# Optimization experiments

Measured on AMD Instinct MI355X. Metric: run time of the kernel, lower is better.

The kernel has to match this reference:

```python
import jax, jax.numpy as jnp
import numpy as np

B, C, H, W = 32, 64, 32, 32
N = H * W  # 1024 spatial positions


def setup_inputs() -> dict:
    key = jax.random.key(0)
    ks = jax.random.split(key, 7)
    s_c = 1.0 / np.sqrt(C)
    s_n = 1.0 / np.sqrt(N)
    return {
        "x": jax.random.normal(ks[0], (B, C, H, W), dtype=jnp.float32),
        "w_phi": jax.random.normal(ks[1], (C, C), dtype=jnp.float32) * s_c,
        "w_theta": jax.random.normal(ks[2], (C, C), dtype=jnp.float32) * s_c,
        "w_g": jax.random.normal(ks[3], (C, C), dtype=jnp.float32) * s_c,
        "w_mask": jax.random.normal(ks[4], (C, C), dtype=jnp.float32) * s_c,
        "w_mv": jax.random.normal(ks[5], (C, C), dtype=jnp.float32) * s_c,
        "w_mk": jax.random.normal(ks[6], (N, N), dtype=jnp.float32) * s_n,
    }


def reference(x, w_phi, w_theta, w_g, w_mask, w_mv, w_mk):
    b, c, h, w = x.shape
    n = h * w
    xf = x.reshape(b, c, n)  # [b, c, N]
    # 1x1 convs == channel GEMMs (weight layout [out, in])
    phi = jnp.einsum("oc,bcn->bon", w_phi, xf)      # [b, c, N]
    theta = jnp.einsum("oc,bcn->bno", w_theta, xf)  # [b, N, c]
    g = jnp.einsum("oc,bcn->bno", w_g, xf)          # [b, N, c]
    # mv: Linear(c, c) on last dim of g  (y = g @ W^T)
    g = jnp.einsum("bnc,dc->bnd", g, w_mv)
    # theta @ phi -> [b, N, N]
    att = jnp.einsum("bnc,bcm->bnm", theta, phi)
    # mk: Linear(N, N) on last dim
    att = jnp.einsum("bnm,km->bnk", att, w_mk)
    # softmax over dim=1 (rows of the NxN map)
    att = jax.nn.softmax(att, axis=1)
    # att @ g -> [b, N, c]
    out = jnp.einsum("bnm,bmc->bnc", att, g)
    out = out.transpose(0, 2, 1).reshape(b, c, h, w)
    mask = jnp.einsum("oc,bchw->bohw", w_mask, out)
    return mask + x
```

## Files before the change

kernel.cpp:

```cpp
#include <hip/hip_runtime.h>

#define BB 32
#define CC 64
#define NN 1024

typedef __attribute__((ext_vector_type(8))) short bf8;
typedef __attribute__((ext_vector_type(4))) float f4;
typedef __attribute__((ext_vector_type(4))) unsigned short us4;

__device__ __forceinline__ unsigned short f2bf(float f) {
    unsigned u = __float_as_uint(f);
    return (unsigned short)((u + 0x7fffu + ((u >> 16) & 1u)) >> 16);
}
__device__ __forceinline__ float bf2f(unsigned short u) {
    return __uint_as_float(((unsigned)u) << 16);
}

#define MFMA(a, b, c) __builtin_amdgcn_mfma_f32_16x16x32_bf16(a, b, c, 0, 0, 0)

#define GLDS(g, l)                                                              \
    __builtin_amdgcn_global_load_lds(                                           \
        (const __attribute__((address_space(1))) void*)(g),                     \
        (__attribute__((address_space(3))) void*)(l), 16, 0, 0)

__device__ __forceinline__ void swz512(int i, int& b, int& t0) {
    int gid = (i & 7) * 64 + (i >> 3);
    b = gid >> 4;
    t0 = (gid & 15) * 64;
}

__global__ void k0_prep(const float* __restrict__ w_mv, const float* __restrict__ w_g,
                        const float* __restrict__ w_theta, const float* __restrict__ w_phi,
                        const float* __restrict__ w_mask,
                        unsigned short* __restrict__ wcat_bf,
                        unsigned short* __restrict__ wmask_bf) {
    int idx = blockIdx.x * 256 + threadIdx.x;
    int d = idx >> 6, e = idx & 63;
    float acc = 0.f;
    for (int c = 0; c < 64; ++c) acc += w_mv[d * 64 + c] * w_g[c * 64 + e];
    wcat_bf[idx] = f2bf(w_theta[idx]);
    wcat_bf[4096 + idx] = f2bf(w_phi[idx]);
    wcat_bf[8192 + idx] = f2bf(acc);
    wmask_bf[idx] = f2bf(w_mask[idx]);
}

__global__ __launch_bounds__(256, 4) void k1_channel(const float* __restrict__ x,
                                                     const float* __restrict__ w_mk,
                                                     const unsigned short* __restrict__ wcat,
                                                     unsigned short* __restrict__ theta_nc,
                                                     unsigned short* __restrict__ phi_cm,
                                                     unsigned short* __restrict__ g2_cm,
                                                     unsigned short* __restrict__ wmk_bf) {
    __shared__ __align__(16) unsigned short xT[32][72];
    int b = blockIdx.y;
    int n0 = blockIdx.x * 32;
    int tid = threadIdx.x;
    int w = tid >> 6, lane = tid & 63, l16 = lane & 15, q = lane >> 4;
    size_t bo = (size_t)b * CC * NN;
    {
        int wi = (b * 32 + blockIdx.x) * 1024 + tid * 4;
        float4 wv = *(const float4*)(w_mk + wi);
        us4 wr;
        wr.x = f2bf(wv.x); wr.y = f2bf(wv.y); wr.z = f2bf(wv.z); wr.w = f2bf(wv.w);
        *(us4*)(wmk_bf + wi) = wr;
    }
#pragma unroll
    for (int i = 0; i < 2; ++i) {
        int f = i * 1024 + tid * 4;
        int c = f >> 5, n = f & 31;
        float4 v = *(const float4*)(x + bo + (size_t)c * NN + n0 + n);
        xT[n + 0][c] = f2bf(v.x);
        xT[n + 1][c] = f2bf(v.y);
        xT[n + 2][c] = f2bf(v.z);
        xT[n + 3][c] = f2bf(v.w);
    }
    __syncthreads();
    bf8 bF[2][2];
#pragma unroll
    for (int ct = 0; ct < 2; ++ct) {
        bF[ct][0] = *(const bf8*)&xT[ct * 16 + l16][q * 8];
        bF[ct][1] = *(const bf8*)&xT[ct * 16 + l16][32 + q * 8];
    }
#pragma unroll
    for (int rt = 0; rt < 3; ++rt) {
        int R = w * 48 + rt * 16;
        const unsigned short* wa = wcat + (R + l16) * 64 + q * 8;
        bf8 a0 = *(const bf8*)wa;
        bf8 a1 = *(const bf8*)(wa + 32);
        int which = R >> 6, rb = R & 63;
#pragma unroll
        for (int ct = 0; ct < 2; ++ct) {
            f4 acc = {0.f, 0.f, 0.f, 0.f};
            acc = MFMA(a0, bF[ct][0], acc);
            acc = MFMA(a1, bF[ct][1], acc);
            int n = n0 + ct * 16 + l16;
            if (which == 0) {
                us4 t;
                t.x = f2bf(acc[0]); t.y = f2bf(acc[1]);
                t.z = f2bf(acc[2]); t.w = f2bf(acc[3]);
                *(us4*)&theta_nc[bo + (size_t)n * 64 + rb + q * 4] = t;
            } else {
                unsigned short* dst = (which == 1 ? phi_cm : g2_cm) + bo;
#pragma unroll
                for (int r = 0; r < 4; ++r)
                    dst[(size_t)(rb + q * 4 + r) * NN + n] = f2bf(acc[r]);
            }
        }
    }
}

__global__ __launch_bounds__(512, 4) void k23_phi2_stats(
    const unsigned short* __restrict__ phi_cm,
    const unsigned short* __restrict__ wmk_bf,
    const unsigned short* __restrict__ theta_nc,
    unsigned short* __restrict__ phi2t,
    float* __restrict__ sinv) {
    __shared__ __align__(16) unsigned short bT[2][4096];
    __shared__ __align__(16) unsigned short pT[64][72];
    __shared__ float sred[8][32];
    int b, k0;
    swz512(blockIdx.x, b, k0);
    int tid = threadIdx.x;
    int w = tid >> 6, lane = tid & 63, l16 = lane & 15, q = lane >> 4;
    size_t bo = (size_t)b * CC * NN;
    int srow = w * 8 + (lane >> 3);
    int scol = ((lane & 7) ^ (lane >> 3)) * 8;

    int ks = w & 3, ch = w >> 2;
    const unsigned short* gsrc = phi_cm + bo + (size_t)srow * NN + scol;
    const unsigned short* arow = wmk_bf + (size_t)(k0 + ks * 16 + l16) * NN + q * 8;
    f4 acc[2];
    acc[0] = (f4){0.f, 0.f, 0.f, 0.f};
    acc[1] = (f4){0.f, 0.f, 0.f, 0.f};
    bf8 aC0 = *(const bf8*)(arow);
    bf8 aC1 = *(const bf8*)(arow + 32);
    GLDS(gsrc, &bT[0][w * 512]);
    __syncthreads();
#pragma unroll 2
    for (int mc = 0; mc < 16; ++mc) {
        const unsigned short* bTc = bT[mc & 1];
        bf8 aN0 = aC0, aN1 = aC1;
        if (mc < 15) {
            int mn = (mc + 1) * 64;
            aN0 = *(const bf8*)(arow + mn);
            aN1 = *(const bf8*)(arow + mn + 32);
            GLDS(gsrc + mn, &bT[(mc + 1) & 1][w * 512]);
            asm volatile("s_waitcnt vmcnt(3)" ::: "memory");
        } else {
            asm volatile("s_waitcnt vmcnt(0)" ::: "memory");
        }
        __builtin_amdgcn_s_barrier();
        __builtin_amdgcn_sched_barrier(0);
#pragma unroll
        for (int t = 0; t < 2; ++t) {
            int row = (ch * 2 + t) * 16 + l16;
            int sw = (row & 7) * 8;
            bf8 b0 = *(const bf8*)&bTc[row * 64 + ((q * 8) ^ sw)];
            bf8 b1 = *(const bf8*)&bTc[row * 64 + ((32 + q * 8) ^ sw)];
            acc[t] = MFMA(aC0, b0, acc[t]);
            acc[t] = MFMA(aC1, b1, acc[t]);
        }
        __builtin_amdgcn_s_barrier();
        __builtin_amdgcn_sched_barrier(0);
        aC0 = aN0;
        aC1 = aN1;
    }
    unsigned short* prow = phi2t + bo;
#pragma unroll
    for (int t = 0; t < 2; ++t) {
        int ccol = (ch * 2 + t) * 16 + l16;
#pragma unroll
        for (int r = 0; r < 4; ++r) {
            int krow = ks * 16 + q * 4 + r;
            unsigned short v = f2bf(acc[t][r]);
            pT[krow][ccol] = v;
            prow[(size_t)(k0 + krow) * 64 + ccol] = v;
        }
    }

    int rg = w & 3, th = w >> 2;
    const unsigned short* thsrc = theta_nc + bo + (size_t)srow * 64 + scol;
    GLDS(thsrc, &bT[0][w * 512]);
    __syncthreads();
    bf8 pF[2][2];
#pragma unroll
    for (int t = 0; t < 2; ++t)
#pragma unroll
        for (int kc = 0; kc < 2; ++kc)
            pF[t][kc] = *(const bf8*)&pT[(th * 2 + t) * 16 + l16][kc * 32 + q * 8];
    float s[2] = {0.f, 0.f};
#pragma unroll 2
    for (int nc = 0; nc < 16; ++nc) {
        const unsigned short* tTc = bT[nc & 1];
        if (nc < 15) {
            GLDS(thsrc + (nc + 1) * 4096, &bT[(nc + 1) & 1][w * 512]);
            asm volatile("s_waitcnt vmcnt(1)" ::: "memory");
        } else {
            asm volatile("s_waitcnt vmcnt(0)" ::: "memory");
        }
        __builtin_amdgcn_s_barrier();
        __builtin_amdgcn_sched_barrier(0);
        int r = rg * 16 + l16;
        int sw = (r & 7);
        bf8 a0 = *(const bf8*)&tTc[r * 64 + ((q ^ sw) * 8)];
        bf8 a1 = *(const bf8*)&tTc[r * 64 + (((4 + q) ^ sw) * 8)];
#pragma unroll
        for (int t = 0; t < 2; ++t) {
            f4 at = {0.f, 0.f, 0.f, 0.f};
            at = MFMA(a0, pF[t][0], at);
            at = MFMA(a1, pF[t][1], at);
            s[t] += __expf(at[0]) + __expf(at[1]) + __expf(at[2]) + __expf(at[3]);
        }
        __builtin_amdgcn_s_barrier();
        __builtin_amdgcn_sched_barrier(0);
    }
#pragma unroll
    for (int t = 0; t < 2; ++t) {
        s[t] += __shfl_xor(s[t], 16, 64);
        s[t] += __shfl_xor(s[t], 32, 64);
    }
    if (q == 0) {
        sred[w][l16] = s[0];
        sred[w][16 + l16] = s[1];
    }
    __syncthreads();
    if (tid < 64) {
        int th2 = tid >> 5, rem = tid & 31;
        float S = sred[th2 * 4 + 0][rem] + sred[th2 * 4 + 1][rem] +
                  sred[th2 * 4 + 2][rem] + sred[th2 * 4 + 3][rem];
        sinv[(size_t)b * NN + k0 + tid] = 1.f / S;
    }
}

__global__ __launch_bounds__(512, 4) void k4_out(const unsigned short* __restrict__ theta_nc,
                                                 const unsigned short* __restrict__ phi2t,
                                                 const unsigned short* __restrict__ g2_cm,
                                                 const float* __restrict__ sinv,
                                                 const unsigned short* __restrict__ wmask_bf,
                                                 const float* __restrict__ x,
                                                 float* __restrict__ out) {
    __shared__ __align__(16) unsigned short smem[23040];
    float* svs_l = (float*)(smem + 20992);
    int b, n0;
    swz512(blockIdx.x, b, n0);
    int tid = threadIdx.x;
    int w = tid >> 6, lane = tid & 63, l16 = lane & 15, q = lane >> 4;
    int ws = w & 3, ph = w >> 2;
    int nl = ws * 16 + l16;
    size_t bo = (size_t)b * CC * NN;
    int srow = w * 8 + (lane >> 3);
    int scol = ((lane & 7) ^ (lane >> 3)) * 8;
    const unsigned short* p2b = phi2t + bo;
    const unsigned short* g2b = g2_cm + bo;
    if (tid < 256) *(f4*)&svs_l[tid * 4] = *(const f4*)(sinv + (size_t)b * NN + tid * 4);
    bf8 thB[2];
#pragma unroll
    for (int kc = 0; kc < 2; ++kc)
        thB[kc] = *(const bf8*)(theta_nc + bo + (size_t)(n0 + nl) * 64 + kc * 32 + q * 8);
    f4 accO[4];
#pragma unroll
    for (int ct = 0; ct < 4; ++ct) accO[ct] = (f4){0.f, 0.f, 0.f, 0.f};
    GLDS(p2b + (size_t)srow * 64 + scol, smem + w * 512);
    GLDS(g2b + (size_t)srow * NN + scol, smem + 4096 + w * 512);
    __syncthreads();
#pragma unroll 2
    for (int mc = 0; mc < 16; ++mc) {
        unsigned short* aT = smem + (mc & 1) * 8192;
        unsigned short* gT = aT + 4096;
        if (mc < 15) {
            int mn = (mc + 1) * 64;
            unsigned short* aN = smem + ((mc + 1) & 1) * 8192;
            GLDS(p2b + (size_t)(mn + srow) * 64 + scol, aN + w * 512);
            GLDS(g2b + (size_t)srow * NN + mn + scol, aN + 4096 + w * 512);
            asm volatile("s_waitcnt vmcnt(2)" ::: "memory");
        } else {
            asm volatile("s_waitcnt vmcnt(0)" ::: "memory");
        }
        __builtin_amdgcn_s_barrier();
        __builtin_amdgcn_sched_barrier(0);
        int m0 = mc * 64;
        unsigned short* Pr = smem + 16384 + nl * 72 + ph * 32;
        int swz = (l16 & 7) * 8;
#pragma unroll
        for (int mrr = 0; mrr < 2; ++mrr) {
            int rowA = ph * 32 + mrr * 16 + l16;
            bf8 a0 = *(const bf8*)&aT[rowA * 64 + ((q * 8) ^ swz)];
            bf8 a1 = *(const bf8*)&aT[rowA * 64 + ((32 + q * 8) ^ swz)];
            f4 at = {0.f, 0.f, 0.f, 0.f};
            at = MFMA(a0, thB[0], at);
            at = MFMA(a1, thB[1], at);
            f4 sv = *(const f4*)&svs_l[m0 + ph * 32 + mrr * 16 + q * 4];
            us4 pk;
            pk.x = f2bf(__expf(at[0]) * sv[0]);
            pk.y = f2bf(__expf(at[1]) * sv[1]);
            pk.z = f2bf(__expf(at[2]) * sv[2]);
            pk.w = f2bf(__expf(at[3]) * sv[3]);
            *(us4*)&Pr[mrr * 16 + q * 4] = pk;
        }
        bf8 pF = *(const bf8*)&Pr[q * 8];
#pragma unroll
        for (int ct = 0; ct < 4; ++ct) {
            int rowG = ct * 16 + l16;
            bf8 g0 = *(const bf8*)&gT[rowG * 64 + (((ph * 32) + q * 8) ^ swz)];
            accO[ct] = MFMA(g0, pF, accO[ct]);
        }
        __builtin_amdgcn_s_barrier();
        __builtin_amdgcn_sched_barrier(0);
    }
    float* o_red = (float*)smem;
    unsigned short* o_lds = smem + 8704;
    if (ph == 1) {
#pragma unroll
        for (int ct = 0; ct < 4; ++ct)
#pragma unroll
            for (int r = 0; r < 4; ++r) o_red[(ct * 16 + q * 4 + r) * 68 + nl] = accO[ct][r];
    }
    __syncthreads();
    if (ph == 0) {
#pragma unroll
        for (int ct = 0; ct < 4; ++ct) {
            us4 ov;
            ov.x = f2bf(accO[ct][0] + o_red[(ct * 16 + q * 4 + 0) * 68 + nl]);
            ov.y = f2bf(accO[ct][1] + o_red[(ct * 16 + q * 4 + 1) * 68 + nl]);
            ov.z = f2bf(accO[ct][2] + o_red[(ct * 16 + q * 4 + 2) * 68 + nl]);
            ov.w = f2bf(accO[ct][3] + o_red[(ct * 16 + q * 4 + 3) * 68 + nl]);
            *(us4*)&o_lds[nl * 72 + ct * 16 + q * 4] = ov;
        }
    }
    __syncthreads();
    bf8 oB0 = *(const bf8*)&o_lds[nl * 72 + q * 8];
    bf8 oB1 = *(const bf8*)&o_lds[nl * 72 + 32 + q * 8];
#pragma unroll
    for (int t2 = 0; t2 < 2; ++t2) {
        int tr = ph * 2 + t2;
        const unsigned short* wa = wmask_bf + (tr * 16 + l16) * 64 + q * 8;
        bf8 w0 = *(const bf8*)wa;
        bf8 w1 = *(const bf8*)(wa + 32);
        f4 accF = {0.f, 0.f, 0.f, 0.f};
        accF = MFMA(w0, oB0, accF);
        accF = MFMA(w1, oB1, accF);
#pragma unroll
        for (int r = 0; r < 4; ++r) {
            size_t ix = bo + (size_t)(tr * 16 + q * 4 + r) * NN + n0 + nl;
            out[ix] = accF[r] + x[ix];
        }
    }
}

extern "C" void kernel_launch(void* const* d_in, const int* in_sizes, int n_in,
                              void* d_out, int out_size, void* d_ws, size_t ws_size,
                              hipStream_t stream) {
    const float* x       = (const float*)d_in[0];
    const float* w_phi   = (const float*)d_in[1];
    const float* w_theta = (const float*)d_in[2];
    const float* w_g     = (const float*)d_in[3];
    const float* w_mask  = (const float*)d_in[4];
    const float* w_mv    = (const float*)d_in[5];
    const float* w_mk    = (const float*)d_in[6];
    float* out = (float*)d_out;

    const size_t CN = (size_t)BB * CC * NN;
    char* p = (char*)d_ws;
    unsigned short* theta_nc = (unsigned short*)p; p += CN * 2;
    unsigned short* phi_cm = (unsigned short*)p;   p += CN * 2;
    unsigned short* g2_cm = (unsigned short*)p;    p += CN * 2;
    float* sinv = (float*)p;                       p += CN * 2;
    unsigned short* phi2t = (unsigned short*)p;    p += CN * 2;
    unsigned short* wmk_bf = (unsigned short*)p;   p += (size_t)NN * NN * 2;
    unsigned short* wcat_bf = (unsigned short*)p;  p += 192 * 64 * 2;
    unsigned short* wmask_bf = (unsigned short*)p; p += 4096 * 2;

    k0_prep<<<16, 256, 0, stream>>>(w_mv, w_g, w_theta, w_phi, w_mask,
                                    wcat_bf, wmask_bf);
    k1_channel<<<dim3(32, BB), 256, 0, stream>>>(x, w_mk, wcat_bf, theta_nc,
                                                 phi_cm, g2_cm, wmk_bf);
    k23_phi2_stats<<<512, 512, 0, stream>>>(phi_cm, wmk_bf, theta_nc, phi2t, sinv);
    k4_out<<<512, 512, 0, stream>>>(theta_nc, phi2t, g2_cm, sinv, wmask_bf, x, out);
}
```

Measured before the change: 132.5 us.

## Split k23 into 1024 blocks of 256 threads covering 32 k-rows each

The phi2/softmax-stats kernel now processes 32 output rows per block with 4 waves instead of 64 rows with 8 waves, launching twice as many blocks. Each wave loads two LDS chunks per stage and covers two row halves in the stats loop. The goal is better spreading across CUs and less tail imbalance, at the cost of reloading the full phi and theta tiles per block, which doubles global and LDS traffic for those operands.

```diff
diff --git a/kernel.cpp b/kernel.cpp
--- a/kernel.cpp
+++ b/kernel.cpp
@@ -27,6 +27,11 @@
     int gid = (i & 7) * 64 + (i >> 3);
     b = gid >> 4;
     t0 = (gid & 15) * 64;
+}
+__device__ __forceinline__ void swz1024(int i, int& b, int& t0) {
+    int gid = (i & 7) * 128 + (i >> 3);
+    b = gid >> 5;
+    t0 = (gid & 31) * 32;
 }
 
 __global__ void k0_prep(const float* __restrict__ w_mv, const float* __restrict__ w_g,
@@ -109,43 +114,46 @@
     }
 }
 
-__global__ __launch_bounds__(512, 4) void k23_phi2_stats(
+__global__ __launch_bounds__(256, 4) void k23_phi2_stats(
     const unsigned short* __restrict__ phi_cm,
     const unsigned short* __restrict__ wmk_bf,
     const unsigned short* __restrict__ theta_nc,
     unsigned short* __restrict__ phi2t,
     float* __restrict__ sinv) {
     __shared__ __align__(16) unsigned short bT[2][4096];
-    __shared__ __align__(16) unsigned short pT[64][72];
-    __shared__ float sred[8][32];
+    __shared__ __align__(16) unsigned short pT[32][72];
+    __shared__ float sred[4][16];
     int b, k0;
-    swz512(blockIdx.x, b, k0);
+    swz1024(blockIdx.x, b, k0);
     int tid = threadIdx.x;
     int w = tid >> 6, lane = tid & 63, l16 = lane & 15, q = lane >> 4;
     size_t bo = (size_t)b * CC * NN;
-    int srow = w * 8 + (lane >> 3);
+    int srow = w * 16 + (lane >> 3);
     int scol = ((lane & 7) ^ (lane >> 3)) * 8;
 
-    int ks = w & 3, ch = w >> 2;
-    const unsigned short* gsrc = phi_cm + bo + (size_t)srow * NN + scol;
-    const unsigned short* arow = wmk_bf + (size_t)(k0 + ks * 16 + l16) * NN + q * 8;
+    int ks = w & 1, ch = w >> 1;
+    const unsigned short* ga0 = phi_cm + bo + (size_t)srow * NN + scol;
+    const unsigned short* ga1 = ga0 + (size_t)8 * NN;
+    const unsigned short* krow = wmk_bf + (size_t)(k0 + ks * 16 + l16) * NN + q * 8;
     f4 acc[2];
     acc[0] = (f4){0.f, 0.f, 0.f, 0.f};
     acc[1] = (f4){0.f, 0.f, 0.f, 0.f};
-    bf8 aC0 = *(const bf8*)(arow);
-    bf8 aC1 = *(const bf8*)(arow + 32);
-    GLDS(gsrc, &bT[0][w * 512]);
+    bf8 aC0 = *(const bf8*)(krow);
+    bf8 aC1 = *(const bf8*)(krow + 32);
+    GLDS(ga0, &bT[0][w * 1024]);
+    GLDS(ga1, &bT[0][w * 1024 + 512]);
     __syncthreads();
 #pragma unroll 2
     for (int mc = 0; mc < 16; ++mc) {
-        const unsigned short* bTc = bT[mc & 1];
+        const unsigned short* buf = bT[mc & 1];
         bf8 aN0 = aC0, aN1 = aC1;
         if (mc < 15) {
             int mn = (mc + 1) * 64;
-            aN0 = *(const bf8*)(arow + mn);
-            aN1 = *(const bf8*)(arow + mn + 32);
-            GLDS(gsrc + mn, &bT[(mc + 1) & 1][w * 512]);
-            asm volatile("s_waitcnt vmcnt(3)" ::: "memory");
+            aN0 = *(const bf8*)(krow + mn);
+            aN1 = *(const bf8*)(krow + mn + 32);
+            GLDS(ga0 + mn, &bT[(mc + 1) & 1][w * 1024]);
+            GLDS(ga1 + mn, &bT[(mc + 1) & 1][w * 1024 + 512]);
+            asm volatile("s_waitcnt vmcnt(4)" ::: "memory");
         } else {
             asm volatile("s_waitcnt vmcnt(0)" ::: "memory");
         }
@@ -155,8 +163,8 @@
         for (int t = 0; t < 2; ++t) {
             int row = (ch * 2 + t) * 16 + l16;
             int sw = (row & 7) * 8;
-            bf8 b0 = *(const bf8*)&bTc[row * 64 + ((q * 8) ^ sw)];
-            bf8 b1 = *(const bf8*)&bTc[row * 64 + ((32 + q * 8) ^ sw)];
+            bf8 b0 = *(const bf8*)&buf[row * 64 + ((q * 8) ^ sw)];
+            bf8 b1 = *(const bf8*)&buf[row * 64 + ((32 + q * 8) ^ sw)];
             acc[t] = MFMA(aC0, b0, acc[t]);
             acc[t] = MFMA(aC1, b1, acc[t]);
         }
@@ -171,63 +179,57 @@
         int ccol = (ch * 2 + t) * 16 + l16;
 #pragma unroll
         for (int r = 0; r < 4; ++r) {
-            int krow = ks * 16 + q * 4 + r;
+            int krow2 = ks * 16 + q * 4 + r;
             unsigned short v = f2bf(acc[t][r]);
-            pT[krow][ccol] = v;
-            prow[(size_t)(k0 + krow) * 64 + ccol] = v;
-        }
-    }
-
-    int rg = w & 3, th = w >> 2;
-    const unsigned short* thsrc = theta_nc + bo + (size_t)srow * 64 + scol;
-    GLDS(thsrc, &bT[0][w * 512]);
-    __syncthreads();
-    bf8 pF[2][2];
-#pragma unroll
-    for (int t = 0; t < 2; ++t)
-#pragma unroll
-        for (int kc = 0; kc < 2; ++kc)
-            pF[t][kc] = *(const bf8*)&pT[(th * 2 + t) * 16 + l16][kc * 32 + q * 8];
-    float s[2] = {0.f, 0.f};
+            pT[krow2][ccol] = v;
+            prow[(size_t)(k0 + krow2) * 64 + ccol] = v;
+        }
+    }
+
+    int rg = w & 1, th = w >> 1;
+    const unsigned short* gt0 = theta_nc + bo + (size_t)srow * 64 + scol;
+    const unsigned short* gt1 = gt0 + 8 * 64;
+    GLDS(gt0, &bT[0][w * 1024]);
+    GLDS(gt1, &bT[0][w * 1024 + 512]);
+    __syncthreads();
+    bf8 pF[2];
+#pragma unroll
+    for (int kc = 0; kc < 2; ++kc)
+        pF[kc] = *(const bf8*)&pT[th * 16 + l16][kc * 32 + q * 8];
+    float s = 0.f;
 #pragma unroll 2
     for (int nc = 0; nc < 16; ++nc) {
-        const unsigned short* tTc = bT[nc & 1];
+        const unsigned short* buf = bT[nc & 1];
         if (nc < 15) {
-            GLDS(thsrc + (nc + 1) * 4096, &bT[(nc + 1) & 1][w * 512]);
-            asm volatile("s_waitcnt vmcnt(1)" ::: "memory");
+            GLDS(gt0 + (nc + 1) * 4096, &bT[(nc + 1) & 1][w * 1024]);
+            GLDS(gt1 + (nc + 1) * 4096, &bT[(nc + 1) & 1][w * 1024 + 512]);
+            asm volatile("s_waitcnt vmcnt(2)" ::: "memory");
         } else {
             asm volatile("s_waitcnt vmcnt(0)" ::: "memory");
         }
         __builtin_amdgcn_s_barrier();
         __builtin_amdgcn_sched_barrier(0);
-        int r = rg * 16 + l16;
-        int sw = (r & 7);
-        bf8 a0 = *(const bf8*)&tTc[r * 64 + ((q ^ sw) * 8)];
-        bf8 a1 = *(const bf8*)&tTc[r * 64 + (((4 + q) ^ sw) * 8)];
-#pragma unroll
-        for (int t = 0; t < 2; ++t) {
+#pragma unroll
+        for (int half = 0; half < 2; ++half) {
+            int r = half * 32 + rg * 16 + l16;
+            int sw = (r & 7);
+            bf8 a0 = *(const bf8*)&buf[r * 64 + ((q ^ sw) * 8)];
+            bf8 a1 = *(const bf8*)&buf[r * 64 + (((4 + q) ^ sw) * 8)];
             f4 at = {0.f, 0.f, 0.f, 0.f};
-            at = MFMA(a0, pF[t][0], at);
-            at = MFMA(a1, pF[t][1], at);
-            s[t] += __expf(at[0]) + __expf(at[1]) + __expf(at[2]) + __expf(at[3]);
-        }
-        __builtin_amdgcn_s_barrier();
-        __builtin_amdgcn_sched_barrier(0);
-    }
-#pragma unroll
-    for (int t = 0; t < 2; ++t) {
-        s[t] += __shfl_xor(s[t], 16, 64);
-        s[t] += __shfl_xor(s[t], 32, 64);
-    }
-    if (q == 0) {
-        sred[w][l16] = s[0];
-        sred[w][16 + l16] = s[1];
-    }
-    __syncthreads();
-    if (tid < 64) {
-        int th2 = tid >> 5, rem = tid & 31;
-        float S = sred[th2 * 4 + 0][rem] + sred[th2 * 4 + 1][rem] +
-                  sred[th2 * 4 + 2][rem] + sred[th2 * 4 + 3][rem];
+            at = MFMA(a0, pF[0], at);
+            at = MFMA(a1, pF[1], at);
+            s += __expf(at[0]) + __expf(at[1]) + __expf(at[2]) + __expf(at[3]);
+        }
+        __builtin_amdgcn_s_barrier();
+        __builtin_amdgcn_sched_barrier(0);
+    }
+    s += __shfl_xor(s, 16, 64);
+    s += __shfl_xor(s, 32, 64);
+    if (q == 0) sred[w][l16] = s;
+    __syncthreads();
+    if (tid < 32) {
+        int th2 = tid >> 4, rem = tid & 15;
+        float S = sred[th2 * 2 + 0][rem] + sred[th2 * 2 + 1][rem];
         sinv[(size_t)b * NN + k0 + tid] = 1.f / S;
     }
 }
@@ -374,6 +376,6 @@
                                     wcat_bf, wmask_bf);
     k1_channel<<<dim3(32, BB), 256, 0, stream>>>(x, w_mk, wcat_bf, theta_nc,
                                                  phi_cm, g2_cm, wmk_bf);
-    k23_phi2_stats<<<512, 512, 0, stream>>>(phi_cm, wmk_bf, theta_nc, phi2t, sinv);
+    k23_phi2_stats<<<1024, 256, 0, stream>>>(phi_cm, wmk_bf, theta_nc, phi2t, sinv);
     k4_out<<<512, 512, 0, stream>>>(theta_nc, phi2t, g2_cm, sinv, wmask_bf, x, out);
 }
```

Result: no change. 133.2 us (+0.5%).
